# Optimization experiments

Hardware: AMD Instinct MI355X
Metric: run time of the kernel (lower is better)

Reference implementation:

```python
import jax, jax.numpy as jnp
import numpy as np

B, T, N = 8, 12, 256
T_IN = S_IN = P_IN = 32
O_IN = 64
HID = 64
OUT = 64
HEADS = 4


def setup_inputs() -> dict:
    key = jax.random.key(0)
    ks = jax.random.split(key, 26)
    f = lambda k, shape: jax.random.normal(k, shape, jnp.float32) * 0.05
    return {
        'x': jax.random.normal(ks[0], (B, T, N, O_IN), jnp.float32),
        'adj': jax.random.randint(ks[1], (B, T, N, N), 0, 2, jnp.int32),
        'te': jax.random.normal(ks[2], (B, T, T_IN), jnp.float32),
        'se': jax.random.normal(ks[3], (N, S_IN), jnp.float32),
        'pe': jax.random.normal(ks[4], (N, P_IN), jnp.float32),
        # SPGAT linear layers
        'Wt': f(ks[5], (T_IN, HID)), 'bt': f(ks[6], (HID,)),
        'Ws': f(ks[7], (S_IN, HID)), 'bs': f(ks[8], (HID,)),
        'Wp': f(ks[9], (P_IN, HID)), 'bp': f(ks[10], (HID,)),
        'Wfc': f(ks[11], (HID, OUT)), 'bfc': f(ks[12], (OUT,)),
        'Wout': f(ks[13], (2 * OUT, OUT)), 'bout': f(ks[14], (OUT,)),
        # GAT layer 1 (heads=HEADS, concat)
        'W1': f(ks[15], (O_IN, HEADS * HID)), 'b1': f(ks[16], (HEADS * HID,)),
        'a1_src': f(ks[17], (HEADS, HID)), 'a1_dst': f(ks[18], (HEADS, HID)),
        # GAT layer 2 (heads=1)
        'W2': f(ks[19], (HEADS * HID, OUT)), 'b2': f(ks[20], (OUT,)),
        'a2_src': f(ks[21], (1, OUT)), 'a2_dst': f(ks[22], (1, OUT)),
    }


def _gat_conv(h, mask, W, b, a_src, a_dst, heads):
    # h: [B,T,N,Fin]; mask: [B,T,N,N] bool, mask[...,i,j] => edge i->j (coo row=src, col=dst)
    d = W.shape[1] // heads
    hp = (h @ W).reshape(h.shape[0], h.shape[1], h.shape[2], heads, d)  # [B,T,N,H,d]
    es = jnp.einsum('btnhd,hd->bthn', hp, a_src)  # source attention logits
    ed = jnp.einsum('btnhd,hd->bthn', hp, a_dst)  # target attention logits
    # scores[...,h,i,j] = leaky(es_i + ed_j), softmax over sources i per target j
    sc = jax.nn.leaky_relu(es[..., :, None] + ed[..., None, :], 0.2)  # [B,T,H,N,N]
    sc = jnp.where(mask[:, :, None, :, :], sc, jnp.float32(-1e9))
    alpha = jax.nn.softmax(sc, axis=-2)
    out = jnp.einsum('bthij,btihd->btjhd', alpha, hp)  # aggregate at target j
    return out.reshape(h.shape[0], h.shape[1], h.shape[2], heads * d) + b


def reference(x, adj, te, se, pe, Wt, bt, Ws, bs, Wp, bp, Wfc, bfc, Wout, bout,
              W1, b1, a1_src, a1_dst, W2, b2, a2_src, a2_dst):
    mask = adj != 0
    t = (te @ Wt + bt) @ Wfc + bfc          # [B,T,OUT]
    s = (se @ Ws + bs) @ Wfc + bfc          # [N,OUT]
    p = (pe @ Wp + bp) @ Wfc + bfc          # [N,OUT]
    sp = jnp.concatenate([s, p], axis=-1) @ Wout + bout  # [N,OUT]
    st = sp[None, None, :, :] + t[:, :, None, :]         # [B,T,N,OUT]
    h = jax.nn.elu(_gat_conv(x, mask, W1, b1, a1_src, a1_dst, HEADS))
    od = _gat_conv(h, mask, W2, b2, a2_src, a2_dst, 1)   # [B,T,N,OUT]
    return jnp.concatenate([od, st], axis=-1) @ Wout + bout
```

## Files before the change

kernel.cpp:

```cpp
#include <hip/hip_runtime.h>
#include <hip/hip_bf16.h>
#include <cstdint>

#define NNODE 256
#define NBT   96
#define LOG2E 1.4426950408889634f

typedef __attribute__((ext_vector_type(8))) short short8;
typedef __attribute__((ext_vector_type(4))) float f32x4;

__device__ __forceinline__ unsigned pack_bf16x2(float a, float b) {
  unsigned ua = __float_as_uint(a);
  unsigned ub = __float_as_uint(b);
  unsigned ra = (ua + 0x7FFFu + ((ua >> 16) & 1u)) >> 16;
  unsigned rb = ((ub + 0x7FFFu + ((ub >> 16) & 1u)) >> 16) << 16;
  return ra | rb;
}
__device__ __forceinline__ unsigned short bf16_rn(float a) {
  unsigned ua = __float_as_uint(a);
  return (unsigned short)((ua + 0x7FFFu + ((ua >> 16) & 1u)) >> 16);
}
__device__ __forceinline__ float blo(unsigned u) { return __uint_as_float(u << 16); }
__device__ __forceinline__ float bhi(unsigned u) { return __uint_as_float(u & 0xFFFF0000u); }

__global__ __launch_bounds__(256) void pack_mask_kernel(const int* __restrict__ adj,
                                                        unsigned* __restrict__ mb) {
  const int bt = blockIdx.x, w = blockIdx.y, j = threadIdx.x;
  const int* a = adj + (size_t)bt * NNODE * NNODE + (size_t)w * 32 * NNODE;
  unsigned v = 0;
#pragma unroll
  for (int b = 0; b < 32; ++b)
    v |= (a[b * NNODE + j] != 0 ? 1u : 0u) << b;
  mb[((size_t)bt * 8 + w) * 256 + j] = v;
}

__global__ __launch_bounds__(64) void embed_kernel(
    const float* __restrict__ te, const float* __restrict__ se, const float* __restrict__ pe,
    const float* __restrict__ Wt, const float* __restrict__ bt_,
    const float* __restrict__ Ws, const float* __restrict__ bs_,
    const float* __restrict__ Wp, const float* __restrict__ bp_,
    const float* __restrict__ Wfc, const float* __restrict__ bfc,
    const float* __restrict__ Wout, const float* __restrict__ bout,
    float* __restrict__ tW, float* __restrict__ spW) {
  const int j = threadIdx.x;
  __shared__ float A[64], Bv[64], C[64], D[64];
  const int blk = blockIdx.x;
  if (blk < NBT) {
    const int row = blk;
    float h = bt_[j];
    for (int k = 0; k < 32; ++k) h += te[row * 32 + k] * Wt[k * 64 + j];
    A[j] = h;
    __syncthreads();
    float tv = bfc[j];
    for (int k = 0; k < 64; ++k) tv += A[k] * Wfc[k * 64 + j];
    Bv[j] = tv;
    __syncthreads();
    float tw = bout[j];
    for (int d = 0; d < 64; ++d) tw += Bv[d] * Wout[(64 + d) * 64 + j];
    tW[row * 64 + j] = tw;
  } else {
    const int n = blk - NBT;
    float sh = bs_[j], ph = bp_[j];
    for (int k = 0; k < 32; ++k) {
      sh += se[n * 32 + k] * Ws[k * 64 + j];
      ph += pe[n * 32 + k] * Wp[k * 64 + j];
    }
    A[j] = sh; Bv[j] = ph;
    __syncthreads();
    float sv = bfc[j], pv = bfc[j];
    for (int k = 0; k < 64; ++k) {
      sv += A[k] * Wfc[k * 64 + j];
      pv += Bv[k] * Wfc[k * 64 + j];
    }
    C[j] = sv; D[j] = pv;
    __syncthreads();
    float spv = bout[j];
    for (int k = 0; k < 64; ++k)
      spv += C[k] * Wout[k * 64 + j] + D[k] * Wout[(64 + k) * 64 + j];
    __syncthreads();
    A[j] = spv;
    __syncthreads();
    float spw = 0.f;
    for (int d = 0; d < 64; ++d) spw += A[d] * Wout[(64 + d) * 64 + j];
    spW[n * 64 + j] = spw;
  }
}

__global__ __launch_bounds__(256) void prep_kernel(
    const float* __restrict__ Wout, const float* __restrict__ W1,
    const float* __restrict__ W2, unsigned short* __restrict__ WoT,
    unsigned short* __restrict__ W1T, unsigned short* __restrict__ W2T) {
  const int tid = threadIdx.x;
  if (blockIdx.x == 0) {
    {
      const int c = tid >> 2, d0 = (tid & 3) * 16;
#pragma unroll
      for (int i = 0; i < 16; ++i)
        WoT[c * 64 + d0 + i] = bf16_rn(Wout[(size_t)(d0 + i) * 64 + c]);
    }
    const int k = tid;
#pragma unroll
    for (int d = 0; d < 64; ++d)
      W2T[d * 256 + k] = bf16_rn(W2[(size_t)k * 64 + d]);
  } else {
    const int hd = tid;
    unsigned u[32];
#pragma unroll
    for (int p = 0; p < 32; ++p) {
      float a = W1[(size_t)(2 * p) * 256 + hd];
      float b = W1[(size_t)(2 * p + 1) * 256 + hd];
      u[p] = pack_bf16x2(a, b);
    }
    unsigned* o = (unsigned*)(W1T + (size_t)hd * 64);
#pragma unroll
    for (int p = 0; p < 8; ++p) {
      uint4 v;
      v.x = u[4 * p + 0]; v.y = u[4 * p + 1];
      v.z = u[4 * p + 2]; v.w = u[4 * p + 3];
      *reinterpret_cast<uint4*>(o + 4 * p) = v;
    }
  }
}

__global__ __launch_bounds__(256) void feat1_kernel(
    const float* __restrict__ x, const unsigned* __restrict__ W1Tu,
    unsigned short* __restrict__ hpT1) {
  const int head = blockIdx.x, bt = blockIdx.y, tid = threadIdx.x;
  __shared__ unsigned xb[256][36];
  __shared__ unsigned w1t[64][36];

  {
    const float* xrow = x + ((size_t)bt * NNODE + tid) * 64;
    unsigned u[32];
#pragma unroll
    for (int p = 0; p < 16; ++p) {
      float4 v = reinterpret_cast<const float4*>(xrow)[p];
      u[2 * p] = pack_bf16x2(v.x, v.y);
      u[2 * p + 1] = pack_bf16x2(v.z, v.w);
    }
#pragma unroll
    for (int p = 0; p < 8; ++p) {
      uint4 v; v.x = u[4 * p]; v.y = u[4 * p + 1]; v.z = u[4 * p + 2]; v.w = u[4 * p + 3];
      *reinterpret_cast<uint4*>(&xb[tid][4 * p]) = v;
    }
  }
  {
    const int r = tid >> 2, c0 = (tid & 3) * 8;
    const unsigned* src = W1Tu + ((size_t)(head * 64 + r) * 32) + c0;
    *reinterpret_cast<uint4*>(&w1t[r][c0]) = *reinterpret_cast<const uint4*>(src);
    *reinterpret_cast<uint4*>(&w1t[r][c0 + 4]) = *reinterpret_cast<const uint4*>(src + 4);
  }
  __syncthreads();

  const int lane = tid & 63, wv = tid >> 6;
  const int m = lane & 15, q = lane >> 4;
  const f32x4 z4 = {0.f, 0.f, 0.f, 0.f};
  f32x4 cf[4][4];
#pragma unroll
  for (int mt = 0; mt < 4; ++mt)
#pragma unroll
    for (int nt = 0; nt < 4; ++nt) cf[mt][nt] = z4;

#pragma unroll
  for (int kt = 0; kt < 2; ++kt) {
    short8 af[4], bf[4];
#pragma unroll
    for (int mt = 0; mt < 4; ++mt)
      af[mt] = *reinterpret_cast<const short8*>(&w1t[mt * 16 + m][kt * 16 + q * 4]);
#pragma unroll
    for (int nt = 0; nt < 4; ++nt)
      bf[nt] = *reinterpret_cast<const short8*>(&xb[wv * 64 + nt * 16 + m][kt * 16 + q * 4]);
#pragma unroll
    for (int mt = 0; mt < 4; ++mt)
#pragma unroll
      for (int nt = 0; nt < 4; ++nt)
        cf[mt][nt] = __builtin_amdgcn_mfma_f32_16x16x32_bf16(af[mt], bf[nt], cf[mt][nt], 0, 0, 0);
  }

  unsigned short* go = hpT1 + (size_t)(bt * 4 + head) * 16384;
#pragma unroll
  for (int mt = 0; mt < 4; ++mt)
#pragma unroll
    for (int nt = 0; nt < 4; ++nt)
#pragma unroll
      for (int reg = 0; reg < 4; ++reg) {
        const int d = mt * 16 + q * 4 + reg;
        const int n = wv * 64 + nt * 16 + m;
        go[d * 256 + n] = bf16_rn(cf[mt][nt][reg]);
      }
}

__global__ __launch_bounds__(512, 2) void agg1_kernel(
    const unsigned* __restrict__ hpT1u, const unsigned* __restrict__ mbg,
    const float* __restrict__ a1s, const float* __restrict__ a1d,
    const float* __restrict__ b1, unsigned* __restrict__ hgl) {
  const int bt = blockIdx.x, head = blockIdx.y, tid = threadIdx.x;
  __shared__ union U1 {
    unsigned hpT[64][132];
    unsigned short ob[256][72];
  } sm;
  __shared__ unsigned mbs[8 * 256];
  __shared__ float ess[256], eds[256];
  __shared__ float asv[64], adv[64];

  const int bh = bt * 4 + head;
  const unsigned* gh = hpT1u + (size_t)bh * 8192;
#pragma unroll
  for (int c = 0; c < 4; ++c) {
    int i4 = tid + c * 512;
    int row = i4 >> 5, col = (i4 & 31) << 2;
    *reinterpret_cast<uint4*>(&sm.hpT[row][col]) =
        *reinterpret_cast<const uint4*>(&gh[row * 128 + col]);
  }
  *reinterpret_cast<uint4*>(&mbs[tid * 4]) =
      *reinterpret_cast<const uint4*>(&mbg[(size_t)bt * 2048 + tid * 4]);
  if (tid < 64) asv[tid] = a1s[head * 64 + tid];
  else if (tid < 128) adv[tid - 64] = a1d[head * 64 + (tid - 64)];
  __syncthreads();

  {
    const int n = tid & 255;
    const unsigned sh = (n & 1) * 16;
    const float* av = (tid < 256) ? asv : adv;
    float s = 0.f;
#pragma unroll 8
    for (int d = 0; d < 64; ++d) {
      unsigned u = sm.hpT[d][n >> 1];
      s += __uint_as_float((u >> sh) << 16) * av[d];
    }
    if (tid < 256) ess[n] = s * LOG2E;
    else eds[n] = s * LOG2E;
  }
  __syncthreads();

  const int lane = tid & 63, wv = tid >> 6;
  const int m = lane & 15, q = lane >> 4;
  const f32x4 z4 = {0.f, 0.f, 0.f, 0.f};
  f32x4 cacc[2][4], cden[2];
#pragma unroll
  for (int jt = 0; jt < 2; ++jt) {
    cden[jt] = z4;
#pragma unroll
    for (int nt = 0; nt < 4; ++nt) cacc[jt][nt] = z4;
  }
  float edv[2];
#pragma unroll
  for (int jt = 0; jt < 2; ++jt) edv[jt] = eds[(wv * 2 + jt) * 16 + m];
  const short8 ones8 = {(short)0x3F80, (short)0x3F80, (short)0x3F80, (short)0x3F80,
                        (short)0x3F80, (short)0x3F80, (short)0x3F80, (short)0x3F80};

  for (int kt = 0; kt < 8; ++kt) {
    short8 bfr[4];
#pragma unroll
    for (int nt = 0; nt < 4; ++nt)
      bfr[nt] = *reinterpret_cast<const short8*>(&sm.hpT[nt * 16 + m][kt * 16 + q * 4]);
    float e[8];
    *reinterpret_cast<float4*>(&e[0]) = *reinterpret_cast<const float4*>(&ess[kt * 32 + q * 8]);
    *reinterpret_cast<float4*>(&e[4]) = *reinterpret_cast<const float4*>(&ess[kt * 32 + q * 8 + 4]);
#pragma unroll
    for (int jt = 0; jt < 2; ++jt) {
      const int jr = (wv * 2 + jt) * 16 + m;
      const unsigned bits = mbs[kt * 256 + jr] >> (q * 8);
      float pv[8];
#pragma unroll
      for (int r = 0; r < 8; ++r) {
        float sc = e[r] + edv[jt];
        sc = fmaxf(sc, 0.2f * sc);
        pv[r] = ((bits >> r) & 1u) ? exp2f(sc) : 0.f;
      }
      union { unsigned u[4]; short8 s; } A;
#pragma unroll
      for (int h = 0; h < 4; ++h) A.u[h] = pack_bf16x2(pv[2 * h], pv[2 * h + 1]);
#pragma unroll
      for (int nt = 0; nt < 4; ++nt)
        cacc[jt][nt] = __builtin_amdgcn_mfma_f32_16x16x32_bf16(A.s, bfr[nt], cacc[jt][nt], 0, 0, 0);
      cden[jt] = __builtin_amdgcn_mfma_f32_16x16x32_bf16(A.s, ones8, cden[jt], 0, 0, 0);
    }
  }
  __syncthreads();

  float b1v[4];
#pragma unroll
  for (int nt = 0; nt < 4; ++nt) b1v[nt] = b1[head * 64 + nt * 16 + m];
#pragma unroll
  for (int jt = 0; jt < 2; ++jt) {
#pragma unroll
    for (int reg = 0; reg < 4; ++reg) {
      const int j = (wv * 2 + jt) * 16 + q * 4 + reg;
      const float inv = 1.f / fmaxf(cden[jt][reg], 1e-30f);
#pragma unroll
      for (int nt = 0; nt < 4; ++nt) {
        float v = cacc[jt][nt][reg] * inv + b1v[nt];
        v = v > 0.f ? v : expm1f(v);
        sm.ob[j][nt * 16 + m] = bf16_rn(v);
      }
    }
  }
  __syncthreads();
  unsigned* go = hgl + (size_t)bt * NNODE * 128 + head * 32;
#pragma unroll
  for (int c = 0; c < 4; ++c) {
    int i4 = tid + c * 512;
    int j = i4 >> 3, col = (i4 & 7) * 4;
    *reinterpret_cast<uint4*>(&go[(size_t)j * 128 + col]) =
        *reinterpret_cast<const uint4*>(&sm.ob[j][col * 2]);
  }
}

__global__ __launch_bounds__(256, 2) void feat2_kernel(
    const unsigned* __restrict__ hglu, const unsigned* __restrict__ W2Tu,
    unsigned short* __restrict__ hpT2) {
  const int bt = blockIdx.x, ng = blockIdx.y, tid = threadIdx.x;
  __shared__ unsigned hb[64][132];
  __shared__ unsigned w2t[64][132];

#pragma unroll
  for (int c = 0; c < 8; ++c) {
    int i4 = tid + c * 256;
    int row = i4 >> 5, col = (i4 & 31) << 2;
    *reinterpret_cast<uint4*>(&hb[row][col]) =
        *reinterpret_cast<const uint4*>(&hglu[((size_t)bt * 256 + ng * 64 + row) * 128 + col]);
    *reinterpret_cast<uint4*>(&w2t[row][col]) =
        *reinterpret_cast<const uint4*>(&W2Tu[row * 128 + col]);
  }
  __syncthreads();

  const int lane = tid & 63, wv = tid >> 6;
  const int m = lane & 15, q = lane >> 4;
  const f32x4 z4 = {0.f, 0.f, 0.f, 0.f};
  f32x4 cf[4];
#pragma unroll
  for (int mt = 0; mt < 4; ++mt) cf[mt] = z4;

  for (int kt = 0; kt < 8; ++kt) {
    short8 bf = *reinterpret_cast<const short8*>(&hb[wv * 16 + m][kt * 16 + q * 4]);
#pragma unroll
    for (int mt = 0; mt < 4; ++mt) {
      short8 af = *reinterpret_cast<const short8*>(&w2t[mt * 16 + m][kt * 16 + q * 4]);
      cf[mt] = __builtin_amdgcn_mfma_f32_16x16x32_bf16(af, bf, cf[mt], 0, 0, 0);
    }
  }

  unsigned short* go = hpT2 + (size_t)bt * 16384;
#pragma unroll
  for (int mt = 0; mt < 4; ++mt)
#pragma unroll
    for (int reg = 0; reg < 4; ++reg) {
      const int d = mt * 16 + q * 4 + reg;
      const int n = ng * 64 + wv * 16 + m;
      go[d * 256 + n] = bf16_rn(cf[mt][reg]);
    }
}

__global__ __launch_bounds__(512, 2) void agg2_kernel(
    const unsigned* __restrict__ hpT2u, const unsigned* __restrict__ mbg,
    const float* __restrict__ a2s, const float* __restrict__ a2d,
    const float* __restrict__ b2, const unsigned* __restrict__ WoTu,
    const float* __restrict__ spW, const float* __restrict__ tW,
    float* __restrict__ out) {
  const int bt = blockIdx.x, jh = blockIdx.y, tid = threadIdx.x;
  const int jbase = jh * 128;
  __shared__ union U2 {
    unsigned hpT[64][132];
    unsigned short ob[128][72];
  } sm;
  __shared__ unsigned wol[64][36];
  __shared__ unsigned mbs[8 * 128];
  __shared__ float ess[256], eds[128];
  __shared__ float a2sv[64], a2dv[64];

  const unsigned* gh = hpT2u + (size_t)bt * 8192;
#pragma unroll
  for (int c = 0; c < 4; ++c) {
    int i4 = tid + c * 512;
    int row = i4 >> 5, col = (i4 & 31) << 2;
    *reinterpret_cast<uint4*>(&sm.hpT[row][col]) =
        *reinterpret_cast<const uint4*>(&gh[row * 128 + col]);
  }
  {
    int row = tid >> 3, col = (tid & 7) * 4;
    *reinterpret_cast<uint4*>(&wol[row][col]) =
        *reinterpret_cast<const uint4*>(&WoTu[row * 32 + col]);
  }
  if (tid < 256) {
    int w = tid >> 5, col = (tid & 31) * 4;
    *reinterpret_cast<uint4*>(&mbs[w * 128 + col]) =
        *reinterpret_cast<const uint4*>(&mbg[(size_t)bt * 2048 + w * 256 + jbase + col]);
  }
  if (tid >= 384 && tid < 448) a2sv[tid - 384] = a2s[tid - 384];
  else if (tid >= 448) a2dv[tid - 448] = a2d[tid - 448];
  __syncthreads();

  if (tid < 256) {
    const int n = tid;
    const unsigned sh = (n & 1) * 16;
    float s = 0.f;
#pragma unroll 8
    for (int d = 0; d < 64; ++d) {
      unsigned u = sm.hpT[d][n >> 1];
      s += __uint_as_float((u >> sh) << 16) * a2sv[d];
    }
    ess[n] = s * LOG2E;
  } else if (tid < 384) {
    const int jl = tid - 256;
    const int n = jbase + jl;
    const unsigned sh = (n & 1) * 16;
    float s = 0.f;
#pragma unroll 8
    for (int d = 0; d < 64; ++d) {
      unsigned u = sm.hpT[d][n >> 1];
      s += __uint_as_float((u >> sh) << 16) * a2dv[d];
    }
    eds[jl] = s * LOG2E;
  }
  __syncthreads();

  const int lane = tid & 63, wv = tid >> 6;
  const int m = lane & 15, q = lane >> 4;
  const f32x4 z4 = {0.f, 0.f, 0.f, 0.f};
  f32x4 cacc[4], cden = z4;
#pragma unroll
  for (int nt = 0; nt < 4; ++nt) cacc[nt] = z4;
  const float edv = eds[wv * 16 + m];
  const short8 ones8 = {(short)0x3F80, (short)0x3F80, (short)0x3F80, (short)0x3F80,
                        (short)0x3F80, (short)0x3F80, (short)0x3F80, (short)0x3F80};

  for (int kt = 0; kt < 8; ++kt) {
    short8 bfr[4];
#pragma unroll
    for (int nt = 0; nt < 4; ++nt)
      bfr[nt] = *reinterpret_cast<const short8*>(&sm.hpT[nt * 16 + m][kt * 16 + q * 4]);
    float e[8];
    *reinterpret_cast<float4*>(&e[0]) = *reinterpret_cast<const float4*>(&ess[kt * 32 + q * 8]);
    *reinterpret_cast<float4*>(&e[4]) = *reinterpret_cast<const float4*>(&ess[kt * 32 + q * 8 + 4]);
    const unsigned bits = mbs[kt * 128 + wv * 16 + m] >> (q * 8);
    float pv[8];
#pragma unroll
    for (int r = 0; r < 8; ++r) {
      float sc = e[r] + edv;
      sc = fmaxf(sc, 0.2f * sc);
      pv[r] = ((bits >> r) & 1u) ? exp2f(sc) : 0.f;
    }
    union { unsigned u[4]; short8 s; } A;
#pragma unroll
    for (int h = 0; h < 4; ++h) A.u[h] = pack_bf16x2(pv[2 * h], pv[2 * h + 1]);
#pragma unroll
    for (int nt = 0; nt < 4; ++nt)
      cacc[nt] = __builtin_amdgcn_mfma_f32_16x16x32_bf16(A.s, bfr[nt], cacc[nt], 0, 0, 0);
    cden = __builtin_amdgcn_mfma_f32_16x16x32_bf16(A.s, ones8, cden, 0, 0, 0);
  }
  __syncthreads();

  float b2v[4];
#pragma unroll
  for (int nt = 0; nt < 4; ++nt) b2v[nt] = b2[nt * 16 + m];
#pragma unroll
  for (int reg = 0; reg < 4; ++reg) {
    const int jl = wv * 16 + q * 4 + reg;
    const float inv = 1.f / fmaxf(cden[reg], 1e-30f);
#pragma unroll
    for (int nt = 0; nt < 4; ++nt)
      sm.ob[jl][nt * 16 + m] = bf16_rn(cacc[nt][reg] * inv + b2v[nt]);
  }
  __syncthreads();

  f32x4 c2[4];
#pragma unroll
  for (int ct = 0; ct < 4; ++ct) c2[ct] = z4;
#pragma unroll
  for (int kt2 = 0; kt2 < 2; ++kt2) {
    short8 a2f = *reinterpret_cast<const short8*>(&sm.ob[wv * 16 + m][kt2 * 32 + q * 8]);
#pragma unroll
    for (int ct = 0; ct < 4; ++ct) {
      short8 bw = *reinterpret_cast<const short8*>(&wol[ct * 16 + m][kt2 * 16 + q * 4]);
      c2[ct] = __builtin_amdgcn_mfma_f32_16x16x32_bf16(a2f, bw, c2[ct], 0, 0, 0);
    }
  }
  float tWv[4];
#pragma unroll
  for (int ct = 0; ct < 4; ++ct) tWv[ct] = tW[bt * 64 + ct * 16 + m];
#pragma unroll
  for (int reg = 0; reg < 4; ++reg) {
    const int j = jbase + wv * 16 + q * 4 + reg;
#pragma unroll
    for (int ct = 0; ct < 4; ++ct) {
      const int cc = ct * 16 + m;
      out[((size_t)bt * NNODE + j) * 64 + cc] =
          c2[ct][reg] + spW[j * 64 + cc] + tWv[ct];
    }
  }
}

extern "C" void kernel_launch(void* const* d_in, const int* in_sizes, int n_in,
                              void* d_out, int out_size, void* d_ws, size_t ws_size,
                              hipStream_t stream) {
  const float* x    = (const float*)d_in[0];
  const int*   adj  = (const int*)d_in[1];
  const float* te   = (const float*)d_in[2];
  const float* se   = (const float*)d_in[3];
  const float* pe   = (const float*)d_in[4];
  const float* Wt   = (const float*)d_in[5];
  const float* bt_  = (const float*)d_in[6];
  const float* Ws   = (const float*)d_in[7];
  const float* bs_  = (const float*)d_in[8];
  const float* Wp   = (const float*)d_in[9];
  const float* bp_  = (const float*)d_in[10];
  const float* Wfc  = (const float*)d_in[11];
  const float* bfc  = (const float*)d_in[12];
  const float* Wout = (const float*)d_in[13];
  const float* bout = (const float*)d_in[14];
  const float* W1   = (const float*)d_in[15];
  const float* b1   = (const float*)d_in[16];
  const float* a1s  = (const float*)d_in[17];
  const float* a1d  = (const float*)d_in[18];
  const float* W2   = (const float*)d_in[19];
  const float* b2   = (const float*)d_in[20];
  const float* a2s  = (const float*)d_in[21];
  const float* a2d  = (const float*)d_in[22];

  char* ws = (char*)d_ws;
  unsigned*       mb   = (unsigned*)(ws);
  float*          tW   = (float*)(ws + 786432);
  float*          spW  = (float*)(ws + 811008);
  unsigned short* WoT  = (unsigned short*)(ws + 876544);
  unsigned short* W1T  = (unsigned short*)(ws + 884736);
  unsigned short* W2T  = (unsigned short*)(ws + 917504);
  unsigned short* hpT  = (unsigned short*)(ws + 950272);
  unsigned*       hgl  = (unsigned*)(ws + 13533184);

  pack_mask_kernel<<<dim3(NBT, 8), 256, 0, stream>>>(adj, mb);
  embed_kernel<<<NBT + NNODE, 64, 0, stream>>>(te, se, pe, Wt, bt_, Ws, bs_,
                                               Wp, bp_, Wfc, bfc, Wout, bout, tW, spW);
  prep_kernel<<<2, 256, 0, stream>>>(Wout, W1, W2, WoT, W1T, W2T);
  feat1_kernel<<<dim3(4, NBT), 256, 0, stream>>>(x, (const unsigned*)W1T, hpT);
  agg1_kernel<<<dim3(NBT, 4), 512, 0, stream>>>((const unsigned*)hpT, mb, a1s, a1d,
                                                b1, hgl);
  feat2_kernel<<<dim3(NBT, 4), 256, 0, stream>>>(hgl, (const unsigned*)W2T, hpT);
  agg2_kernel<<<dim3(NBT, 2), 512, 0, stream>>>((const unsigned*)hpT, mb, a2s, a2d,
                                                b2, (const unsigned*)WoT, spW, tW,
                                                (float*)d_out);
}
```

Baseline: 183.0 us.

## Fuse layer-1 feature projection into attention aggregation, split targets across blocks

Merges feat1 and agg1 into a single kernel that computes the bf16 projection of x by W1 in shared memory, then runs the attention softmax and aggregation directly from LDS. This removes the global write and re-read of the projected features and one kernel launch. Each block now handles half the target nodes (grid z=2), doubling block count for better occupancy. In exchange, each of the two half-blocks recomputes the full projection and the source logits.

```diff
diff --git a/kernel.cpp b/kernel.cpp
--- a/kernel.cpp
+++ b/kernel.cpp
@@ -20,8 +20,6 @@
   unsigned ua = __float_as_uint(a);
   return (unsigned short)((ua + 0x7FFFu + ((ua >> 16) & 1u)) >> 16);
 }
-__device__ __forceinline__ float blo(unsigned u) { return __uint_as_float(u << 16); }
-__device__ __forceinline__ float bhi(unsigned u) { return __uint_as_float(u & 0xFFFF0000u); }
 
 __global__ __launch_bounds__(256) void pack_mask_kernel(const int* __restrict__ adj,
                                                         unsigned* __restrict__ mb) {
@@ -122,14 +120,22 @@
   }
 }
 
-__global__ __launch_bounds__(256) void feat1_kernel(
+__global__ __launch_bounds__(512, 2) void fused1_kernel(
     const float* __restrict__ x, const unsigned* __restrict__ W1Tu,
-    unsigned short* __restrict__ hpT1) {
-  const int head = blockIdx.x, bt = blockIdx.y, tid = threadIdx.x;
-  __shared__ unsigned xb[256][36];
+    const unsigned* __restrict__ mbg, const float* __restrict__ a1s,
+    const float* __restrict__ a1d, const float* __restrict__ b1,
+    unsigned* __restrict__ hgl) {
+  const int bt = blockIdx.x, head = blockIdx.y, z = blockIdx.z, tid = threadIdx.x;
+  __shared__ union U {
+    unsigned xb[256][36];
+    unsigned hpT[64][132];
+    unsigned short ob[128][72];
+  } sm;
   __shared__ unsigned w1t[64][36];
-
-  {
+  __shared__ unsigned mbs[1024];
+  __shared__ float ess[256], eds[128], asv[64], adv[64];
+
+  if (tid < 256) {
     const float* xrow = x + ((size_t)bt * NNODE + tid) * 64;
     unsigned u[32];
 #pragma unroll
@@ -141,111 +147,94 @@
 #pragma unroll
     for (int p = 0; p < 8; ++p) {
       uint4 v; v.x = u[4 * p]; v.y = u[4 * p + 1]; v.z = u[4 * p + 2]; v.w = u[4 * p + 3];
-      *reinterpret_cast<uint4*>(&xb[tid][4 * p]) = v;
-    }
-  }
-  {
-    const int r = tid >> 2, c0 = (tid & 3) * 8;
-    const unsigned* src = W1Tu + ((size_t)(head * 64 + r) * 32) + c0;
-    *reinterpret_cast<uint4*>(&w1t[r][c0]) = *reinterpret_cast<const uint4*>(src);
-    *reinterpret_cast<uint4*>(&w1t[r][c0 + 4]) = *reinterpret_cast<const uint4*>(src + 4);
+      *reinterpret_cast<uint4*>(&sm.xb[tid][4 * p]) = v;
+    }
+    const int w = tid >> 5, col = (tid & 31) * 4;
+    *reinterpret_cast<uint4*>(&mbs[w * 128 + col]) =
+        *reinterpret_cast<const uint4*>(&mbg[(size_t)bt * 2048 + w * 256 + z * 128 + col]);
+  } else {
+    const int tt = tid - 256;
+#pragma unroll
+    for (int c = 0; c < 2; ++c) {
+      const int idx = tt * 2 + c;
+      const int r = idx >> 3, c4 = (idx & 7) * 4;
+      *reinterpret_cast<uint4*>(&w1t[r][c4]) =
+          *reinterpret_cast<const uint4*>(&W1Tu[(size_t)(head * 64 + r) * 32 + c4]);
+    }
+    if (tt < 64) asv[tt] = a1s[head * 64 + tt];
+    else if (tt < 128) adv[tt - 64] = a1d[head * 64 + (tt - 64)];
   }
   __syncthreads();
 
   const int lane = tid & 63, wv = tid >> 6;
   const int m = lane & 15, q = lane >> 4;
   const f32x4 z4 = {0.f, 0.f, 0.f, 0.f};
-  f32x4 cf[4][4];
+
+  f32x4 cf[4][2];
 #pragma unroll
   for (int mt = 0; mt < 4; ++mt)
 #pragma unroll
-    for (int nt = 0; nt < 4; ++nt) cf[mt][nt] = z4;
-
+    for (int nt = 0; nt < 2; ++nt) cf[mt][nt] = z4;
 #pragma unroll
   for (int kt = 0; kt < 2; ++kt) {
-    short8 af[4], bf[4];
+    short8 af[4], bf[2];
 #pragma unroll
     for (int mt = 0; mt < 4; ++mt)
       af[mt] = *reinterpret_cast<const short8*>(&w1t[mt * 16 + m][kt * 16 + q * 4]);
 #pragma unroll
-    for (int nt = 0; nt < 4; ++nt)
-      bf[nt] = *reinterpret_cast<const short8*>(&xb[wv * 64 + nt * 16 + m][kt * 16 + q * 4]);
+    for (int nt = 0; nt < 2; ++nt)
+      bf[nt] = *reinterpret_cast<const short8*>(&sm.xb[wv * 32 + nt * 16 + m][kt * 16 + q * 4]);
 #pragma unroll
     for (int mt = 0; mt < 4; ++mt)
 #pragma unroll
-      for (int nt = 0; nt < 4; ++nt)
+      for (int nt = 0; nt < 2; ++nt)
         cf[mt][nt] = __builtin_amdgcn_mfma_f32_16x16x32_bf16(af[mt], bf[nt], cf[mt][nt], 0, 0, 0);
   }
-
-  unsigned short* go = hpT1 + (size_t)(bt * 4 + head) * 16384;
-#pragma unroll
-  for (int mt = 0; mt < 4; ++mt)
-#pragma unroll
-    for (int nt = 0; nt < 4; ++nt)
-#pragma unroll
-      for (int reg = 0; reg < 4; ++reg) {
-        const int d = mt * 16 + q * 4 + reg;
-        const int n = wv * 64 + nt * 16 + m;
-        go[d * 256 + n] = bf16_rn(cf[mt][nt][reg]);
-      }
-}
-
-__global__ __launch_bounds__(512, 2) void agg1_kernel(
-    const unsigned* __restrict__ hpT1u, const unsigned* __restrict__ mbg,
-    const float* __restrict__ a1s, const float* __restrict__ a1d,
-    const float* __restrict__ b1, unsigned* __restrict__ hgl) {
-  const int bt = blockIdx.x, head = blockIdx.y, tid = threadIdx.x;
-  __shared__ union U1 {
-    unsigned hpT[64][132];
-    unsigned short ob[256][72];
-  } sm;
-  __shared__ unsigned mbs[8 * 256];
-  __shared__ float ess[256], eds[256];
-  __shared__ float asv[64], adv[64];
-
-  const int bh = bt * 4 + head;
-  const unsigned* gh = hpT1u + (size_t)bh * 8192;
-#pragma unroll
-  for (int c = 0; c < 4; ++c) {
-    int i4 = tid + c * 512;
-    int row = i4 >> 5, col = (i4 & 31) << 2;
-    *reinterpret_cast<uint4*>(&sm.hpT[row][col]) =
-        *reinterpret_cast<const uint4*>(&gh[row * 128 + col]);
-  }
-  *reinterpret_cast<uint4*>(&mbs[tid * 4]) =
-      *reinterpret_cast<const uint4*>(&mbg[(size_t)bt * 2048 + tid * 4]);
-  if (tid < 64) asv[tid] = a1s[head * 64 + tid];
-  else if (tid < 128) adv[tid - 64] = a1d[head * 64 + (tid - 64)];
   __syncthreads();
 
   {
-    const int n = tid & 255;
+    unsigned short* hpT16 = reinterpret_cast<unsigned short*>(&sm.hpT[0][0]);
+#pragma unroll
+    for (int mt = 0; mt < 4; ++mt)
+#pragma unroll
+      for (int nt = 0; nt < 2; ++nt)
+#pragma unroll
+        for (int reg = 0; reg < 4; ++reg) {
+          const int d = mt * 16 + q * 4 + reg;
+          const int n = wv * 32 + nt * 16 + m;
+          hpT16[d * 264 + n] = bf16_rn(cf[mt][nt][reg]);
+        }
+  }
+  __syncthreads();
+
+  if (tid < 256) {
+    const int n = tid;
     const unsigned sh = (n & 1) * 16;
-    const float* av = (tid < 256) ? asv : adv;
     float s = 0.f;
 #pragma unroll 8
     for (int d = 0; d < 64; ++d) {
       unsigned u = sm.hpT[d][n >> 1];
-      s += __uint_as_float((u >> sh) << 16) * av[d];
-    }
-    if (tid < 256) ess[n] = s * LOG2E;
-    else eds[n] = s * LOG2E;
-  }
-  __syncthreads();
-
-  const int lane = tid & 63, wv = tid >> 6;
-  const int m = lane & 15, q = lane >> 4;
-  const f32x4 z4 = {0.f, 0.f, 0.f, 0.f};
-  f32x4 cacc[2][4], cden[2];
-#pragma unroll
-  for (int jt = 0; jt < 2; ++jt) {
-    cden[jt] = z4;
-#pragma unroll
-    for (int nt = 0; nt < 4; ++nt) cacc[jt][nt] = z4;
-  }
-  float edv[2];
-#pragma unroll
-  for (int jt = 0; jt < 2; ++jt) edv[jt] = eds[(wv * 2 + jt) * 16 + m];
+      s += __uint_as_float((u >> sh) << 16) * asv[d];
+    }
+    ess[n] = s * LOG2E;
+  } else if (tid < 384) {
+    const int jl = tid - 256;
+    const int n = z * 128 + jl;
+    const unsigned sh = (n & 1) * 16;
+    float s = 0.f;
+#pragma unroll 8
+    for (int d = 0; d < 64; ++d) {
+      unsigned u = sm.hpT[d][n >> 1];
+      s += __uint_as_float((u >> sh) << 16) * adv[d];
+    }
+    eds[jl] = s * LOG2E;
+  }
+  __syncthreads();
+
+  f32x4 cacc[4], cden = z4;
+#pragma unroll
+  for (int nt = 0; nt < 4; ++nt) cacc[nt] = z4;
+  const float edv = eds[wv * 16 + m];
   const short8 ones8 = {(short)0x3F80, (short)0x3F80, (short)0x3F80, (short)0x3F80,
                         (short)0x3F80, (short)0x3F80, (short)0x3F80, (short)0x3F80};
 
@@ -257,25 +246,21 @@
     float e[8];
     *reinterpret_cast<float4*>(&e[0]) = *reinterpret_cast<const float4*>(&ess[kt * 32 + q * 8]);
     *reinterpret_cast<float4*>(&e[4]) = *reinterpret_cast<const float4*>(&ess[kt * 32 + q * 8 + 4]);
-#pragma unroll
-    for (int jt = 0; jt < 2; ++jt) {
-      const int jr = (wv * 2 + jt) * 16 + m;
-      const unsigned bits = mbs[kt * 256 + jr] >> (q * 8);
-      float pv[8];
-#pragma unroll
-      for (int r = 0; r < 8; ++r) {
-        float sc = e[r] + edv[jt];
-        sc = fmaxf(sc, 0.2f * sc);
-        pv[r] = ((bits >> r) & 1u) ? exp2f(sc) : 0.f;
-      }
-      union { unsigned u[4]; short8 s; } A;
-#pragma unroll
-      for (int h = 0; h < 4; ++h) A.u[h] = pack_bf16x2(pv[2 * h], pv[2 * h + 1]);
-#pragma unroll
-      for (int nt = 0; nt < 4; ++nt)
-        cacc[jt][nt] = __builtin_amdgcn_mfma_f32_16x16x32_bf16(A.s, bfr[nt], cacc[jt][nt], 0, 0, 0);
-      cden[jt] = __builtin_amdgcn_mfma_f32_16x16x32_bf16(A.s, ones8, cden[jt], 0, 0, 0);
-    }
+    const unsigned bits = mbs[kt * 128 + wv * 16 + m] >> (q * 8);
+    float pv[8];
+#pragma unroll
+    for (int r = 0; r < 8; ++r) {
+      float sc = e[r] + edv;
+      sc = fmaxf(sc, 0.2f * sc);
+      pv[r] = ((bits >> r) & 1u) ? exp2f(sc) : 0.f;
+    }
+    union { unsigned u[4]; short8 s; } A;
+#pragma unroll
+    for (int h = 0; h < 4; ++h) A.u[h] = pack_bf16x2(pv[2 * h], pv[2 * h + 1]);
+#pragma unroll
+    for (int nt = 0; nt < 4; ++nt)
+      cacc[nt] = __builtin_amdgcn_mfma_f32_16x16x32_bf16(A.s, bfr[nt], cacc[nt], 0, 0, 0);
+    cden = __builtin_amdgcn_mfma_f32_16x16x32_bf16(A.s, ones8, cden, 0, 0, 0);
   }
   __syncthreads();
 
@@ -283,27 +268,25 @@
 #pragma unroll
   for (int nt = 0; nt < 4; ++nt) b1v[nt] = b1[head * 64 + nt * 16 + m];
 #pragma unroll
-  for (int jt = 0; jt < 2; ++jt) {
-#pragma unroll
-    for (int reg = 0; reg < 4; ++reg) {
-      const int j = (wv * 2 + jt) * 16 + q * 4 + reg;
-      const float inv = 1.f / fmaxf(cden[jt][reg], 1e-30f);
-#pragma unroll
-      for (int nt = 0; nt < 4; ++nt) {
-        float v = cacc[jt][nt][reg] * inv + b1v[nt];
-        v = v > 0.f ? v : expm1f(v);
-        sm.ob[j][nt * 16 + m] = bf16_rn(v);
-      }
-    }
-  }
-  __syncthreads();
-  unsigned* go = hgl + (size_t)bt * NNODE * 128 + head * 32;
-#pragma unroll
-  for (int c = 0; c < 4; ++c) {
-    int i4 = tid + c * 512;
-    int j = i4 >> 3, col = (i4 & 7) * 4;
-    *reinterpret_cast<uint4*>(&go[(size_t)j * 128 + col]) =
-        *reinterpret_cast<const uint4*>(&sm.ob[j][col * 2]);
+  for (int reg = 0; reg < 4; ++reg) {
+    const int jl = wv * 16 + q * 4 + reg;
+    const float inv = 1.f / fmaxf(cden[reg], 1e-30f);
+#pragma unroll
+    for (int nt = 0; nt < 4; ++nt) {
+      float v = cacc[nt][reg] * inv + b1v[nt];
+      v = v > 0.f ? v : expm1f(v);
+      sm.ob[jl][nt * 16 + m] = bf16_rn(v);
+    }
+  }
+  __syncthreads();
+
+  unsigned* go = hgl + (size_t)bt * 32768 + (size_t)z * 128 * 128 + head * 32;
+#pragma unroll
+  for (int c = 0; c < 2; ++c) {
+    const int idx = tid * 2 + c;
+    const int jl = idx >> 3, c4 = (idx & 7) * 4;
+    *reinterpret_cast<uint4*>(&go[(size_t)jl * 128 + c4]) =
+        *reinterpret_cast<const uint4*>(&sm.ob[jl][c4 * 2]);
   }
 }
 
@@ -532,9 +515,8 @@
   embed_kernel<<<NBT + NNODE, 64, 0, stream>>>(te, se, pe, Wt, bt_, Ws, bs_,
                                                Wp, bp_, Wfc, bfc, Wout, bout, tW, spW);
   prep_kernel<<<2, 256, 0, stream>>>(Wout, W1, W2, WoT, W1T, W2T);
-  feat1_kernel<<<dim3(4, NBT), 256, 0, stream>>>(x, (const unsigned*)W1T, hpT);
-  agg1_kernel<<<dim3(NBT, 4), 512, 0, stream>>>((const unsigned*)hpT, mb, a1s, a1d,
-                                                b1, hgl);
+  fused1_kernel<<<dim3(NBT, 4, 2), 512, 0, stream>>>(x, (const unsigned*)W1T, mb,
+                                                     a1s, a1d, b1, hgl);
   feat2_kernel<<<dim3(NBT, 4), 256, 0, stream>>>(hgl, (const unsigned*)W2T, hpT);
   agg2_kernel<<<dim3(NBT, 2), 512, 0, stream>>>((const unsigned*)hpT, mb, a2s, a2d,
                                                 b2, (const unsigned*)WoT, spW, tW,
```

Result: faster. 168.6 us (-7.9%).
